# Performance work log

Measured on AMD Instinct MI355X. Metric: run time of the kernel, lower is better.

Reference implementation:

```python
import jax, jax.numpy as jnp
import numpy as np

IN_C = 32        # in_channel
CH = IN_C + 3    # first-layer input channel (use_coords=True)
HID = 8
OUT_C = 1
# parameter slicing offsets: w1(35*8) b1(8) w2(8*8) b2(8) w3(8*1) b3(1) = 369
P_COUNT = CH * HID + HID + HID * HID + HID + HID * OUT_C + OUT_C


def setup_inputs() -> dict:
    key = jax.random.key(0)
    k1, k2, k3, k4 = jax.random.split(key, 4)
    num_prop, num_all = 128, 100000
    prop_feats = jax.random.normal(k1, (num_prop, IN_C), dtype=jnp.float32)
    all_features = jax.random.normal(k2, (num_all, CH), dtype=jnp.float32)
    W_dyn = jax.random.normal(k3, (IN_C, P_COUNT), dtype=jnp.float32) * 0.05
    b_dyn = jax.random.normal(k4, (P_COUNT,), dtype=jnp.float32) * 0.05
    return {"prop_feats": prop_feats, "all_features": all_features,
            "W_dyn": W_dyn, "b_dyn": b_dyn}


def reference(prop_feats, all_features, W_dyn, b_dyn):
    P = prop_feats.shape[0]
    params = prop_feats @ W_dyn + b_dyn  # (P, 369)
    s = 0
    def take(n):
        nonlocal s
        out = params[:, s:s + n]
        s += n
        return out
    w1 = take(CH * HID).reshape(P, CH, HID)
    b1 = take(HID)[:, None, :]
    w2 = take(HID * HID).reshape(P, HID, HID)
    b2 = take(HID)[:, None, :]
    w3 = take(HID * OUT_C).reshape(P, HID, OUT_C)
    b3 = take(OUT_C)[:, None, :]
    # layer 1: shared all_features against per-proposal weights (avoids
    # materializing the (P, A, CH) expanded tensor)
    f = jax.nn.relu(jnp.einsum('ac,pch->pah', all_features, w1) + b1)
    # layer 2
    f = jax.nn.relu(jnp.einsum('pah,phk->pak', f, w2) + b2)
    # layer 3 (no activation on last kernel)
    f = jnp.einsum('pah,pho->pao', f, w3) + b3
    return f  # (num_prop, num_all, out_channel)
```

## Files before the change

### kernel.cpp

```cpp
#include <hip/hip_runtime.h>
#include <hip/hip_bf16.h>

#define IN_C  32
#define CH    35
#define P_CNT 369
#define NPAIR 64
#define NALL  100000
#define NTILE 6250
#define TT    8
#define PP    8

#define OW1 0
#define OB1 280
#define OW2 288
#define OB2 352
#define OW3 360
#define OB3 368

#define WS_W1F 0
#define WS_W2F 131072
#define WS_B1F 163840
#define WS_B2F 229376
#define WS_W3F 294912
#define WS_B3F 360448

typedef short  bf16x8 __attribute__((ext_vector_type(8)));
typedef short  bf16x4 __attribute__((ext_vector_type(4)));
typedef float  f32x4  __attribute__((ext_vector_type(4)));

static __device__ inline unsigned short f2bf(float x) {
    union { float f; unsigned u; } v; v.f = x;
    unsigned r = v.u + 0x7FFFu + ((v.u >> 16) & 1u);
    return (unsigned short)(r >> 16);
}

static __device__ inline unsigned pack2bf(float lo, float hi) {
    __hip_bfloat162 h2 = __float22bfloat162_rn(make_float2(lo, hi));
    union { __hip_bfloat162 h; unsigned u; } c; c.h = h2; return c.u;
}

__global__ __launch_bounds__(256) void prep_kernel(
        const float* __restrict__ prop,
        const float* __restrict__ W,
        const float* __restrict__ b,
        char* __restrict__ ws) {
    const int pp  = blockIdx.x;
    const int tid = threadIdx.x;
    __shared__ float P[2][P_CNT];

    for (int idx = tid; idx < 2 * P_CNT; idx += 256) {
        const int pl = (idx >= P_CNT) ? 1 : 0;
        const int j  = idx - pl * P_CNT;
        const float* pr = prop + (size_t)(2 * pp + pl) * IN_C;
        float acc = b[j];
        #pragma unroll
        for (int c = 0; c < IN_C; ++c)
            acc = fmaf(pr[c], W[(size_t)c * P_CNT + j], acc);
        P[pl][j] = acc;
    }
    __syncthreads();

    if (tid >= 64) return;
    const int lane = tid;
    const int g = lane >> 4;
    const int m = lane & 15;

    {
        unsigned short* w1f = (unsigned short*)(ws + WS_W1F);
        const int pl = m >> 3, h = m & 7;
        #pragma unroll
        for (int kh = 0; kh < 2; ++kh)
            #pragma unroll
            for (int j = 0; j < 8; ++j) {
                const int c = kh * 32 + g * 8 + j;
                const float v = (c < CH) ? P[pl][OW1 + c * 8 + h] : 0.f;
                w1f[((size_t)(pp * 2 + kh) * 64 + lane) * 8 + j] = f2bf(v);
            }
    }
    {
        unsigned short* w2f = (unsigned short*)(ws + WS_W2F);
        const int plj = m >> 3, jj = m & 7;
        #pragma unroll
        for (int r = 0; r < 4; ++r) {
            const int colh = g * 4 + r;
            const int ph = colh >> 3, h = colh & 7;
            const float v = (ph == plj) ? P[plj][OW2 + h * 8 + jj] : 0.f;
            w2f[((size_t)pp * 64 + lane) * 4 + r] = f2bf(v);
        }
    }
    {
        float* b1f = (float*)(ws + WS_B1F);
        float* b2f = (float*)(ws + WS_B2F);
        float* w3f = (float*)(ws + WS_W3F);
        #pragma unroll
        for (int r = 0; r < 4; ++r) {
            const int row = g * 4 + r;
            b1f[((size_t)pp * 64 + lane) * 4 + r] = P[row >> 3][OB1 + (row & 7)];
            b2f[((size_t)pp * 64 + lane) * 4 + r] = P[row >> 3][OB2 + (row & 7)];
            w3f[((size_t)pp * 64 + lane) * 4 + r] = P[row >> 3][OW3 + (row & 7)];
        }
    }
    if (lane < 2) ((float*)(ws + WS_B3F))[pp * 2 + lane] = P[lane][OB3];
}

__global__ __launch_bounds__(256, 2) void mlp_kernel(
        const float* __restrict__ allf,
        const char* __restrict__ ws,
        float* __restrict__ out) {
    const int lane = threadIdx.x & 63;
    const int wave = threadIdx.x >> 6;
    const int gidx = blockIdx.x * 4 + wave;
    const int tbase = gidx * TT;
    if (tbase >= NTILE) return;
    const int g   = lane >> 4;
    const int col = lane & 15;

    bf16x8 bf0[TT], bf1[TT];
    #pragma unroll
    for (int tt = 0; tt < TT; ++tt) {
        const int tile = tbase + tt;
        float fv0[8], fv1[8];
        if (tile < NTILE) {
            const float* fr = allf + (size_t)(tile * 16 + col) * CH;
            #pragma unroll
            for (int j = 0; j < 8; ++j) {
                fv0[j] = fr[g * 8 + j];
                const int c1 = 32 + g * 8 + j;
                fv1[j] = (c1 < CH) ? fr[c1] : 0.f;
            }
        } else {
            #pragma unroll
            for (int j = 0; j < 8; ++j) { fv0[j] = 0.f; fv1[j] = 0.f; }
        }
        union { unsigned u[4]; bf16x8 v; } a0, a1;
        #pragma unroll
        for (int q = 0; q < 4; ++q) {
            a0.u[q] = pack2bf(fv0[2 * q], fv0[2 * q + 1]);
            a1.u[q] = pack2bf(fv1[2 * q], fv1[2 * q + 1]);
        }
        bf0[tt] = a0.v; bf1[tt] = a1.v;
    }

    const bf16x8* __restrict__ w1f = (const bf16x8*)(ws + WS_W1F);
    const bf16x4* __restrict__ w2f = (const bf16x4*)(ws + WS_W2F);
    const f32x4*  __restrict__ b1f = (const f32x4*)(ws + WS_B1F);
    const f32x4*  __restrict__ b2f = (const f32x4*)(ws + WS_B2F);
    const f32x4*  __restrict__ w3f = (const f32x4*)(ws + WS_W3F);
    const float2* __restrict__ b3f = (const float2*)(ws + WS_B3F);

    const int ppbase = blockIdx.y * PP;
    #pragma unroll 1
    for (int i = 0; i < PP; ++i) {
        const int pp = ppbase + i;
        const bf16x8 w1a = w1f[(pp * 2 + 0) * 64 + lane];
        const bf16x8 w1b = w1f[(pp * 2 + 1) * 64 + lane];
        const bf16x4 w2v = w2f[pp * 64 + lane];
        const f32x4  b1v = b1f[pp * 64 + lane];
        const f32x4  b2v = b2f[pp * 64 + lane];
        const f32x4  w3v = w3f[pp * 64 + lane];
        const float2 b3v = b3f[pp];

        const size_t pbase_out = (size_t)pp * 2 * NALL + (size_t)tbase * 16 + col;

        #pragma unroll
        for (int tt = 0; tt < TT; ++tt) {
            f32x4 c1 = b1v;
            c1 = __builtin_amdgcn_mfma_f32_16x16x32_bf16(w1a, bf0[tt], c1, 0, 0, 0);
            c1 = __builtin_amdgcn_mfma_f32_16x16x32_bf16(w1b, bf1[tt], c1, 0, 0, 0);

            f32x4 c2;
#if __has_builtin(__builtin_amdgcn_mfma_f32_16x16x16bf16_1k)
            union { unsigned u[2]; bf16x4 v; } pb;
            pb.u[0] = pack2bf(fmaxf(c1[0], 0.f), fmaxf(c1[1], 0.f));
            pb.u[1] = pack2bf(fmaxf(c1[2], 0.f), fmaxf(c1[3], 0.f));
            c2 = __builtin_amdgcn_mfma_f32_16x16x16bf16_1k(w2v, pb.v, b2v, 0, 0, 0);
#else
            float rl[4];
            #pragma unroll
            for (int r = 0; r < 4; ++r) rl[r] = fmaxf(c1[r], 0.f);
            bf16x8 pb8;
            #pragma unroll
            for (int j = 0; j < 8; ++j) {
                const int src = ((2 * g + (j >> 2)) << 4) + col;
                pb8[j] = (short)f2bf(__shfl(rl[j & 3], src, 64));
            }
            bf16x8 w28;
            #pragma unroll
            for (int r = 0; r < 4; ++r) { w28[r] = w2v[r]; w28[r + 4] = 0; }
            c2 = __builtin_amdgcn_mfma_f32_16x16x32_bf16(w28, pb8, b2v, 0, 0, 0);
#endif
            float s;
            s = fmaf(fmaxf(c2[0], 0.f), w3v[0], 0.f);
            s = fmaf(fmaxf(c2[1], 0.f), w3v[1], s);
            s = fmaf(fmaxf(c2[2], 0.f), w3v[2], s);
            s = fmaf(fmaxf(c2[3], 0.f), w3v[3], s);
            const float t = s + __shfl_xor(s, 16, 64);
            if (!(g & 1) && (tbase + tt) < NTILE) {
                const int pl = lane >> 5;
                out[pbase_out + (size_t)pl * NALL + tt * 16] =
                    t + (pl ? b3v.y : b3v.x);
            }
        }
    }
}

extern "C" void kernel_launch(void* const* d_in, const int* in_sizes, int n_in,
                              void* d_out, int out_size, void* d_ws, size_t ws_size,
                              hipStream_t stream) {
    const float* prop = (const float*)d_in[0];
    const float* allf = (const float*)d_in[1];
    const float* W    = (const float*)d_in[2];
    const float* b    = (const float*)d_in[3];
    float* out = (float*)d_out;
    char*  ws  = (char*)d_ws;

    prep_kernel<<<NPAIR, 256, 0, stream>>>(prop, W, b, ws);

    dim3 grid(196, NPAIR / PP);
    mlp_kernel<<<grid, 256, 0, stream>>>(allf, ws, out);
}
```

Before: 128.3 us.

## Keep per-pair weights in registers and stream tiles with next-tile prefetch

The MLP kernel is reorganized so each wave holds the weights for 4 proposal pairs in registers and walks tiles with a grid stride, loading the next tile's features while the current one is computed. The first-layer feature load is simplified to read only the 3 extra channels on one lane group. Launch bounds rise to 3 blocks per CU to raise occupancy. The aim is to hide global load latency and avoid reloading weights per tile. The cost is that features are now re-read by 16 grid rows instead of 8, adding L2 traffic.

```diff
diff --git a/kernel.cpp b/kernel.cpp
--- a/kernel.cpp
+++ b/kernel.cpp
@@ -7,8 +7,8 @@
 #define NPAIR 64
 #define NALL  100000
 #define NTILE 6250
-#define TT    8
-#define PP    8
+#define PP    4
+#define NWX   784
 
 #define OW1 0
 #define OB1 280
@@ -103,77 +103,81 @@
     if (lane < 2) ((float*)(ws + WS_B3F))[pp * 2 + lane] = P[lane][OB3];
 }
 
-__global__ __launch_bounds__(256, 2) void mlp_kernel(
+#define LOAD_TILE(T, O0, O1) do {                                             \
+    const float* fr_ = allf + (size_t)((T) * 16 + col) * CH;                  \
+    const float v0_ = fr_[g * 8 + 0], v1_ = fr_[g * 8 + 1];                   \
+    const float v2_ = fr_[g * 8 + 2], v3_ = fr_[g * 8 + 3];                   \
+    const float v4_ = fr_[g * 8 + 4], v5_ = fr_[g * 8 + 5];                   \
+    const float v6_ = fr_[g * 8 + 6], v7_ = fr_[g * 8 + 7];                   \
+    float e0_ = 0.f, e1_ = 0.f, e2_ = 0.f;                                    \
+    if (g == 0) { e0_ = fr_[32]; e1_ = fr_[33]; e2_ = fr_[34]; }              \
+    union { unsigned u[4]; bf16x8 v; } A0_, A1_;                              \
+    A0_.u[0] = pack2bf(v0_, v1_); A0_.u[1] = pack2bf(v2_, v3_);               \
+    A0_.u[2] = pack2bf(v4_, v5_); A0_.u[3] = pack2bf(v6_, v7_);               \
+    A1_.u[0] = pack2bf(e0_, e1_); A1_.u[1] = pack2bf(e2_, 0.f);               \
+    A1_.u[2] = 0u; A1_.u[3] = 0u;                                             \
+    O0 = A0_.v; O1 = A1_.v; } while (0)
+
+__global__ __launch_bounds__(256, 3) void mlp_kernel(
         const float* __restrict__ allf,
         const char* __restrict__ ws,
         float* __restrict__ out) {
     const int lane = threadIdx.x & 63;
     const int wave = threadIdx.x >> 6;
-    const int gidx = blockIdx.x * 4 + wave;
-    const int tbase = gidx * TT;
-    if (tbase >= NTILE) return;
-    const int g   = lane >> 4;
-    const int col = lane & 15;
-
-    bf16x8 bf0[TT], bf1[TT];
-    #pragma unroll
-    for (int tt = 0; tt < TT; ++tt) {
-        const int tile = tbase + tt;
-        float fv0[8], fv1[8];
-        if (tile < NTILE) {
-            const float* fr = allf + (size_t)(tile * 16 + col) * CH;
-            #pragma unroll
-            for (int j = 0; j < 8; ++j) {
-                fv0[j] = fr[g * 8 + j];
-                const int c1 = 32 + g * 8 + j;
-                fv1[j] = (c1 < CH) ? fr[c1] : 0.f;
-            }
-        } else {
-            #pragma unroll
-            for (int j = 0; j < 8; ++j) { fv0[j] = 0.f; fv1[j] = 0.f; }
-        }
-        union { unsigned u[4]; bf16x8 v; } a0, a1;
-        #pragma unroll
-        for (int q = 0; q < 4; ++q) {
-            a0.u[q] = pack2bf(fv0[2 * q], fv0[2 * q + 1]);
-            a1.u[q] = pack2bf(fv1[2 * q], fv1[2 * q + 1]);
-        }
-        bf0[tt] = a0.v; bf1[tt] = a1.v;
-    }
+    const int wx   = blockIdx.x * 4 + wave;
+    const int g    = lane >> 4;
+    const int col  = lane & 15;
+    const int ppbase = blockIdx.y * PP;
 
     const bf16x8* __restrict__ w1f = (const bf16x8*)(ws + WS_W1F);
     const bf16x4* __restrict__ w2f = (const bf16x4*)(ws + WS_W2F);
     const f32x4*  __restrict__ b1f = (const f32x4*)(ws + WS_B1F);
     const f32x4*  __restrict__ b2f = (const f32x4*)(ws + WS_B2F);
     const f32x4*  __restrict__ w3f = (const f32x4*)(ws + WS_W3F);
-    const float2* __restrict__ b3f = (const float2*)(ws + WS_B3F);
-
-    const int ppbase = blockIdx.y * PP;
-    #pragma unroll 1
+    const float*  __restrict__ b3f = (const float*)(ws + WS_B3F);
+
+    bf16x8 w1a[PP], w1b[PP];
+    bf16x4 w2v[PP];
+    f32x4  b1v[PP], b2v[PP], w3v[PP];
+    float  b3s[PP];
+    #pragma unroll
     for (int i = 0; i < PP; ++i) {
         const int pp = ppbase + i;
-        const bf16x8 w1a = w1f[(pp * 2 + 0) * 64 + lane];
-        const bf16x8 w1b = w1f[(pp * 2 + 1) * 64 + lane];
-        const bf16x4 w2v = w2f[pp * 64 + lane];
-        const f32x4  b1v = b1f[pp * 64 + lane];
-        const f32x4  b2v = b2f[pp * 64 + lane];
-        const f32x4  w3v = w3f[pp * 64 + lane];
-        const float2 b3v = b3f[pp];
-
-        const size_t pbase_out = (size_t)pp * 2 * NALL + (size_t)tbase * 16 + col;
-
-        #pragma unroll
-        for (int tt = 0; tt < TT; ++tt) {
-            f32x4 c1 = b1v;
-            c1 = __builtin_amdgcn_mfma_f32_16x16x32_bf16(w1a, bf0[tt], c1, 0, 0, 0);
-            c1 = __builtin_amdgcn_mfma_f32_16x16x32_bf16(w1b, bf1[tt], c1, 0, 0, 0);
+        w1a[i] = w1f[(pp * 2 + 0) * 64 + lane];
+        w1b[i] = w1f[(pp * 2 + 1) * 64 + lane];
+        w2v[i] = w2f[pp * 64 + lane];
+        b1v[i] = b1f[pp * 64 + lane];
+        b2v[i] = b2f[pp * 64 + lane];
+        w3v[i] = w3f[pp * 64 + lane];
+        b3s[i] = b3f[pp * 2 + (lane >> 5)];
+    }
+    #pragma unroll
+    for (int i = 0; i < PP; ++i)
+        asm volatile("" : "+v"(w1a[i]), "+v"(w1b[i]), "+v"(w2v[i]),
+                          "+v"(b1v[i]), "+v"(b2v[i]), "+v"(w3v[i]));
+
+    if (wx >= NTILE) return;
+
+    bf16x8 cb0, cb1, nb0, nb1;
+    LOAD_TILE(wx, cb0, cb1);
+
+    #pragma unroll 1
+    for (int t = wx; t < NTILE; t += NWX) {
+        const int tn = (t + NWX < NTILE) ? (t + NWX) : t;
+        LOAD_TILE(tn, nb0, nb1);
+
+        #pragma unroll
+        for (int i = 0; i < PP; ++i) {
+            f32x4 c1 = b1v[i];
+            c1 = __builtin_amdgcn_mfma_f32_16x16x32_bf16(w1a[i], cb0, c1, 0, 0, 0);
+            c1 = __builtin_amdgcn_mfma_f32_16x16x32_bf16(w1b[i], cb1, c1, 0, 0, 0);
 
             f32x4 c2;
 #if __has_builtin(__builtin_amdgcn_mfma_f32_16x16x16bf16_1k)
             union { unsigned u[2]; bf16x4 v; } pb;
             pb.u[0] = pack2bf(fmaxf(c1[0], 0.f), fmaxf(c1[1], 0.f));
             pb.u[1] = pack2bf(fmaxf(c1[2], 0.f), fmaxf(c1[3], 0.f));
-            c2 = __builtin_amdgcn_mfma_f32_16x16x16bf16_1k(w2v, pb.v, b2v, 0, 0, 0);
+            c2 = __builtin_amdgcn_mfma_f32_16x16x16bf16_1k(w2v[i], pb.v, b2v[i], 0, 0, 0);
 #else
             float rl[4];
             #pragma unroll
@@ -186,21 +190,22 @@
             }
             bf16x8 w28;
             #pragma unroll
-            for (int r = 0; r < 4; ++r) { w28[r] = w2v[r]; w28[r + 4] = 0; }
-            c2 = __builtin_amdgcn_mfma_f32_16x16x32_bf16(w28, pb8, b2v, 0, 0, 0);
+            for (int r = 0; r < 4; ++r) { w28[r] = w2v[i][r]; w28[r + 4] = 0; }
+            c2 = __builtin_amdgcn_mfma_f32_16x16x32_bf16(w28, pb8, b2v[i], 0, 0, 0);
 #endif
             float s;
-            s = fmaf(fmaxf(c2[0], 0.f), w3v[0], 0.f);
-            s = fmaf(fmaxf(c2[1], 0.f), w3v[1], s);
-            s = fmaf(fmaxf(c2[2], 0.f), w3v[2], s);
-            s = fmaf(fmaxf(c2[3], 0.f), w3v[3], s);
-            const float t = s + __shfl_xor(s, 16, 64);
-            if (!(g & 1) && (tbase + tt) < NTILE) {
+            s = fmaf(fmaxf(c2[0], 0.f), w3v[i][0], 0.f);
+            s = fmaf(fmaxf(c2[1], 0.f), w3v[i][1], s);
+            s = fmaf(fmaxf(c2[2], 0.f), w3v[i][2], s);
+            s = fmaf(fmaxf(c2[3], 0.f), w3v[i][3], s);
+            const float tv = s + __shfl_xor(s, 16, 64);
+            if (!(g & 1)) {
                 const int pl = lane >> 5;
-                out[pbase_out + (size_t)pl * NALL + tt * 16] =
-                    t + (pl ? b3v.y : b3v.x);
+                out[(size_t)((ppbase + i) * 2 + pl) * NALL + t * 16 + col] =
+                    tv + b3s[i];
             }
         }
+        cb0 = nb0; cb1 = nb1;
     }
 }
 
```

Result: slower. 140.7 us (+9.6%).
